# Optimization experiments

Measured on AMD Instinct MI355X. Metric: run time of the kernel, lower is better.

## Reference

```python
import jax, jax.numpy as jnp
import numpy as np

B, L, D = 4, 1024, 512
NST = 16          # d_state
KC = 4            # d_conv
DI = 2 * D        # d_inner (expand=2)
R = (D + 15) // 16  # dt_rank = 32
NM = 4            # mamba instances: 2 layers x (fwd, bwd)


def setup_inputs() -> dict:
    key = jax.random.key(0)
    keys = iter(jax.random.split(key, 64))
    def nrm(shape, s=0.02):
        return jax.random.normal(next(keys), shape, dtype=jnp.float32) * s
    inp = {"x": jax.random.normal(next(keys), (B, L, D), dtype=jnp.float32)}
    # 4 Mamba instances stacked: [layer0_fwd, layer0_bwd, layer1_fwd, layer1_bwd]
    inp["mamba_in_w"] = nrm((NM, 2 * DI, D)); inp["mamba_in_b"] = jnp.zeros((NM, 2 * DI), jnp.float32)
    inp["mamba_conv_w"] = nrm((NM, DI, KC), 0.1); inp["mamba_conv_b"] = jnp.zeros((NM, DI), jnp.float32)
    inp["mamba_xproj_w"] = nrm((NM, R + 2 * NST, DI))
    inp["mamba_dt_w"] = nrm((NM, DI, R)); inp["mamba_dt_b"] = jnp.full((NM, DI), -4.6, jnp.float32)  # softplus -> dt ~ 0.01
    A = jnp.tile(jnp.arange(1, NST + 1, dtype=jnp.float32)[None, :], (DI, 1))  # S4D-real init
    inp["mamba_A_log"] = jnp.tile(jnp.log(A)[None], (NM, 1, 1))
    inp["mamba_D"] = jnp.ones((NM, DI), jnp.float32)
    inp["mamba_out_w"] = nrm((NM, D, DI)); inp["mamba_out_b"] = jnp.zeros((NM, D), jnp.float32)
    # per-BiMambaBlock LayerNorm + FFN params (2 layers)
    inp["ln_w"] = jnp.ones((2, D), jnp.float32); inp["ln_b"] = jnp.zeros((2, D), jnp.float32)
    inp["ffn_ln_w"] = jnp.ones((2, D), jnp.float32); inp["ffn_ln_b"] = jnp.zeros((2, D), jnp.float32)
    inp["ffn_w1"] = nrm((2, 4 * D, D)); inp["ffn_b1"] = jnp.zeros((2, 4 * D), jnp.float32)
    inp["ffn_w2"] = nrm((2, D, 4 * D)); inp["ffn_b2"] = jnp.zeros((2, D), jnp.float32)
    # local conv branches (kernel sizes 5, 7)
    for k in (5, 7):
        inp[f"loc{k}_pw1_w"] = nrm((D, D)); inp[f"loc{k}_pw1_b"] = jnp.zeros((D,), jnp.float32)
        inp[f"loc{k}_dw_w"] = nrm((D, k), 0.1)
        inp[f"loc{k}_pw2_w"] = nrm((D, D)); inp[f"loc{k}_pw2_b"] = jnp.zeros((D,), jnp.float32)
    inp["proj_w"] = nrm((D, 3 * D)); inp["proj_b"] = jnp.zeros((D,), jnp.float32)
    return inp


def _layernorm(x, w, b):
    m = x.mean(-1, keepdims=True)
    v = jnp.var(x, axis=-1, keepdims=True)
    return (x - m) * jax.lax.rsqrt(v + 1e-5) * w + b


def _mamba(u, in_w, in_b, conv_w, conv_b, xp_w, dt_w, dt_b, A_log, Dpar, out_w, out_b):
    # u: [B, L, D]
    xz = u @ in_w.T + in_b
    xm, z = jnp.split(xz, 2, axis=-1)  # each [B, L, DI]
    # causal depthwise conv1d (kernel KC, left pad KC-1) + SiLU
    xt = jnp.swapaxes(xm, 1, 2)  # [B, DI, L]
    xt = jax.lax.conv_general_dilated(xt, conv_w[:, None, :], (1,), [(KC - 1, 0)],
                                      feature_group_count=DI) + conv_b[None, :, None]
    xm = jax.nn.silu(jnp.swapaxes(xt, 1, 2))
    xdb = xm @ xp_w.T  # [B, L, R+2N]
    dt = jax.nn.softplus(xdb[..., :R] @ dt_w.T + dt_b)  # [B, L, DI]
    Bm = xdb[..., R:R + NST]   # [B, L, N]
    Cm = xdb[..., R + NST:]    # [B, L, N]
    A = -jnp.exp(A_log)        # [DI, N]

    def step(h, inp):
        dt_t, B_t, C_t, x_t = inp  # [B,DI],[B,N],[B,N],[B,DI]
        h = h * jnp.exp(dt_t[..., None] * A) + (dt_t * x_t)[..., None] * B_t[:, None, :]
        y = jnp.einsum('bdn,bn->bd', h, C_t)
        return h, y

    h0 = jnp.zeros((u.shape[0], DI, NST), u.dtype)
    xs = (jnp.moveaxis(dt, 1, 0), jnp.moveaxis(Bm, 1, 0),
          jnp.moveaxis(Cm, 1, 0), jnp.moveaxis(xm, 1, 0))
    _, ys = jax.lax.scan(step, h0, xs)  # ys: [L, B, DI]
    y = jnp.moveaxis(ys, 0, 1) + xm * Dpar
    y = y * jax.nn.silu(z)
    return y @ out_w.T + out_b


def _instnorm(h):
    # h: [B, C, L]; InstanceNorm1d default (affine=False, eps=1e-5)
    m = h.mean(-1, keepdims=True)
    v = jnp.var(h, axis=-1, keepdims=True)
    return (h - m) * jax.lax.rsqrt(v + 1e-5)


def _local(x, pw1_w, pw1_b, dw_w, pw2_w, pw2_b, k):
    ht = jnp.swapaxes(x, 1, 2)  # [B, D, L]
    h = jnp.einsum('bcl,dc->bdl', ht, pw1_w) + pw1_b[None, :, None]
    h = jax.nn.silu(_instnorm(h))
    h = jax.lax.conv_general_dilated(h, dw_w[:, None, :], (1,), [(k // 2, k // 2)],
                                     feature_group_count=D)
    h = jax.nn.silu(_instnorm(h))
    h = jnp.einsum('bcl,dc->bdl', h, pw2_w) + pw2_b[None, :, None]
    return jnp.swapaxes(h, 1, 2)


def _forward(x, mamba_in_w, mamba_in_b, mamba_conv_w, mamba_conv_b, mamba_xproj_w,
             mamba_dt_w, mamba_dt_b, mamba_A_log, mamba_D, mamba_out_w, mamba_out_b,
             ln_w, ln_b, ffn_ln_w, ffn_ln_b, ffn_w1, ffn_b1, ffn_w2, ffn_b2,
             loc5_pw1_w, loc5_pw1_b, loc5_dw_w, loc5_pw2_w, loc5_pw2_b,
             loc7_pw1_w, loc7_pw1_b, loc7_dw_w, loc7_pw2_w, loc7_pw2_b,
             proj_w, proj_b):
    mp = (mamba_in_w, mamba_in_b, mamba_conv_w, mamba_conv_b, mamba_xproj_w,
          mamba_dt_w, mamba_dt_b, mamba_A_log, mamba_D, mamba_out_w, mamba_out_b)
    g = x
    for i in range(2):  # num_mamba_layers BiMambaBlocks
        xn = _layernorm(g, ln_w[i], ln_b[i])
        y_fwd = _mamba(xn, *(p[2 * i] for p in mp))
        y_bwd = jnp.flip(_mamba(jnp.flip(xn, 1), *(p[2 * i + 1] for p in mp)), 1)
        g = g + 0.5 * (y_fwd + y_bwd)  # bidir_fusion='mean', residual
        hn = _layernorm(g, ffn_ln_w[i], ffn_ln_b[i])
        h = jax.nn.gelu(hn @ ffn_w1[i].T + ffn_b1[i], approximate=False) @ ffn_w2[i].T + ffn_b2[i]
        g = g + h
    l5 = _local(x, loc5_pw1_w, loc5_pw1_b, loc5_dw_w, loc5_pw2_w, loc5_pw2_b, 5)
    l7 = _local(x, loc7_pw1_w, loc7_pw1_b, loc7_dw_w, loc7_pw2_w, loc7_pw2_b, 7)
    out = jnp.concatenate([g, l5, l7], axis=-1) @ proj_w.T + proj_b  # concat_proj
    return out + x  # lss_residual


def reference(x, mamba_in_w, mamba_in_b, mamba_conv_w, mamba_conv_b, mamba_xproj_w,
              mamba_dt_w, mamba_dt_b, mamba_A_log, mamba_D, mamba_out_w, mamba_out_b,
              ln_w, ln_b, ffn_ln_w, ffn_ln_b, ffn_w1, ffn_b1, ffn_w2, ffn_b2,
              loc5_pw1_w, loc5_pw1_b, loc5_dw_w, loc5_pw2_w, loc5_pw2_b,
              loc7_pw1_w, loc7_pw1_b, loc7_dw_w, loc7_pw2_w, loc7_pw2_b,
              proj_w, proj_b):
    return _forward(x, mamba_in_w, mamba_in_b, mamba_conv_w, mamba_conv_b, mamba_xproj_w,
                    mamba_dt_w, mamba_dt_b, mamba_A_log, mamba_D, mamba_out_w, mamba_out_b,
                    ln_w, ln_b, ffn_ln_w, ffn_ln_b, ffn_w1, ffn_b1, ffn_w2, ffn_b2,
                    loc5_pw1_w, loc5_pw1_b, loc5_dw_w, loc5_pw2_w, loc5_pw2_b,
                    loc7_pw1_w, loc7_pw1_b, loc7_dw_w, loc7_pw2_w, loc7_pw2_b,
                    proj_w, proj_b)
```

## Files before the change

kernel.cpp:

```cpp
#include <hip/hip_runtime.h>
#include <hip/hip_bf16.h>
#include <math.h>

#define BB 4
#define LL 1024
#define DD 512
#define DI 1024
#define NST 16

typedef unsigned short ushort_t;
typedef __attribute__((ext_vector_type(8))) short short8;
typedef __attribute__((ext_vector_type(4))) float f32x4;
typedef __attribute__((ext_vector_type(4))) unsigned short ushort4_t;

__device__ __forceinline__ float silu_f(float x) { return x / (1.f + __expf(-x)); }

__device__ __forceinline__ ushort_t f2bf(float f) {
  union { float f; unsigned u; } v; v.f = f;
  unsigned r = v.u + 0x7fffu + ((v.u >> 16) & 1u);
  return (ushort_t)(r >> 16);
}
__device__ __forceinline__ float bf2f(ushort_t h) {
  union { unsigned u; float f; } v; v.u = ((unsigned)h) << 16;
  return v.f;
}

__device__ __forceinline__ void gl_lds16(const ushort_t* src, ushort_t* dst) {
  __builtin_amdgcn_global_load_lds(
      (const __attribute__((address_space(1))) void*)src,
      (__attribute__((address_space(3))) void*)dst, 16, 0, 0);
}

template <int BN, int ACT, int BIASM, int CMODE, int FLIPA, int FLIPC, int OUTBF, int SPLITK>
__global__ __launch_bounds__(256) void mgemm(
    const ushort_t* __restrict__ A, const ushort_t* __restrict__ Bt,
    const float* __restrict__ bias, void* __restrict__ Cv,
    int K, int lda, int ldb, int ldc, int nreal,
    long sA, long sB, long sC, long sBias, float scale) {
  constexpr int MREP = (BN == 128) ? 4 : 2;
  constexpr int WM = MREP * 16;
  constexpr int NB = BN / 32;
  __shared__ ushort_t As[2][128 * 64];
  __shared__ ushort_t Bs[2][BN * 64];
  const int zz = blockIdx.z;
  const int zdir = (SPLITK == 2) ? (zz >> 2) : zz;
  const ushort_t* Ab;
  const ushort_t* Bb;
  if (SPLITK == 1) {
    Ab = A + (long)zz * K;
    Bb = Bt + (long)zz * K;
  } else if (SPLITK == 2) {
    Ab = A + zdir * sA + (long)(zz & 3) * K;
    Bb = Bt + zdir * sB;
  } else {
    Ab = A + zz * sA;
    Bb = Bt + zz * sB;
  }
  const float* biasp = bias + (long)zdir * sBias;
  const bool flipA = (FLIPA == 1) || (FLIPA == 2 && zdir == 1);
  const bool flipC = (FLIPC == 1) || (FLIPC == 2 && zdir == 1);
  const int flat = blockIdx.y * gridDim.x + blockIdx.x;
  const int nwg = gridDim.x * gridDim.y;
  const int id2 = (flat & 7) * (nwg >> 3) + (flat >> 3);
  const int bm = (id2 / gridDim.x) * 128;
  const int bn = (id2 % gridDim.x) * BN;
  const int tid = threadIdx.x;
  const int wave = tid >> 6, lane = tid & 63;
  const int rlo = lane & 15, q = lane >> 4;
  const int wr = (BN == 128) ? (wave >> 1) : wave;
  const int wc = (BN == 128) ? (wave & 1) : 0;

  f32x4 zero4 = {0.f, 0.f, 0.f, 0.f};
  f32x4 acc[MREP][4];
#pragma unroll
  for (int m = 0; m < MREP; ++m)
#pragma unroll
    for (int n = 0; n < 4; ++n) acc[m][n] = zero4;

  const int srow_off = lane >> 3;
  const int sslot = lane & 7;

#define STAGE_T(bb, k0)                                          \
  do {                                                           \
    _Pragma("unroll") for (int it = 0; it < 4; ++it) {           \
      int c = wave * 4 + it;                                     \
      int row = c * 8 + srow_off;                                \
      int gcol = ((sslot ^ (row & 7)) << 3);                     \
      int gra = bm + row;                                        \
      if (flipA) gra ^= 1023;                                    \
      gl_lds16(Ab + (long)gra * lda + (k0) + gcol, &As[bb][c * 512]); } \
    _Pragma("unroll") for (int it = 0; it < NB; ++it) {          \
      int c = wave * NB + it;                                    \
      int row = c * 8 + srow_off;                                \
      int gcol = ((sslot ^ (row & 7)) << 3);                     \
      gl_lds16(Bb + (long)(bn + row) * ldb + (k0) + gcol, &Bs[bb][c * 512]); } \
  } while (0)

  const int nt = K >> 6;
  STAGE_T(0, 0);
  __syncthreads();
  int cur = 0;
  for (int t = 0; t < nt; ++t) {
    if (t + 1 < nt) STAGE_T(cur ^ 1, (t + 1) * 64);
#pragma unroll
    for (int ks = 0; ks < 2; ++ks) {
      short8 af[MREP], bf[4];
#pragma unroll
      for (int m = 0; m < MREP; ++m) {
        int row = wr * WM + m * 16 + rlo;
        int ch = (ks * 4 + q) ^ (row & 7);
        af[m] = *(const short8*)&As[cur][row * 64 + ch * 8];
      }
#pragma unroll
      for (int n = 0; n < 4; ++n) {
        int row = wc * 64 + n * 16 + rlo;
        int ch = (ks * 4 + q) ^ (row & 7);
        bf[n] = *(const short8*)&Bs[cur][row * 64 + ch * 8];
      }
#pragma unroll
      for (int m = 0; m < MREP; ++m)
#pragma unroll
        for (int n = 0; n < 4; ++n)
          acc[m][n] = __builtin_amdgcn_mfma_f32_16x16x32_bf16(af[m], bf[n], acc[m][n], 0, 0, 0);
    }
    __syncthreads();
    cur ^= 1;
  }
#undef STAGE_T

#pragma unroll
  for (int m = 0; m < MREP; ++m) {
#pragma unroll
    for (int n = 0; n < 4; ++n) {
      int col = bn + wc * 64 + n * 16 + rlo;
      bool cok = (col < nreal);
#pragma unroll
      for (int j = 0; j < 4; ++j) {
        int row = bm + wr * WM + m * 16 + q * 4 + j;
        int orow = flipC ? (row ^ 1023) : row;
        float v = acc[m][n][j];
        if (SPLITK != 1 || zz == 0) {
          if (BIASM == 1) v += biasp[col];
          else if (BIASM == 2) v += biasp[row];
        }
        if (ACT == 1) v = silu_f(v);
        else if (ACT == 2) v = 0.5f * v * (1.f + erff(v * 0.70710678118654752f));
        else if (ACT == 3) v = (v > 20.f) ? v : log1pf(__expf(v));
        if (cok) {
          if (OUTBF) {
            ushort_t* C = (ushort_t*)Cv + (long)zz * sC;
            C[(long)orow * ldc + col] = f2bf(scale * v);
          } else {
            float* C = (float*)Cv + (long)zz * sC;
            if (CMODE == 1) C[(long)orow * ldc + col] += scale * v;
            else C[(long)orow * ldc + col] = scale * v;
          }
        }
      }
    }
  }
}

#define NSEG 10
struct CvtArgs {
  const float* src[NSEG];
  ushort_t* dst[NSEG];
  int start4[NSEG];
};
__global__ __launch_bounds__(256) void cvt_all_kernel(CvtArgs a, int total4) {
  int i = blockIdx.x * 256 + threadIdx.x;
  int stride = gridDim.x * 256;
  for (; i < total4; i += stride) {
    int seg = 0;
#pragma unroll
    for (int s = 1; s < NSEG; ++s)
      if (i >= a.start4[s]) seg = s;
    int off = i - a.start4[seg];
    float4 v = ((const float4*)a.src[seg])[off];
    ushort4_t o;
    o.x = f2bf(v.x); o.y = f2bf(v.y); o.z = f2bf(v.z); o.w = f2bf(v.w);
    *(ushort4_t*)(a.dst[seg] + (long)off * 4) = o;
  }
}

__global__ __launch_bounds__(256) void cvtpad_dtw_kernel(const float* __restrict__ in,
                                                         ushort_t* __restrict__ out) {
  int i = blockIdx.x * 256 + threadIdx.x;
  int k = i & 63;
  int dm = i >> 6;
  out[i] = (k < 32) ? f2bf(in[dm * 32 + k]) : (ushort_t)0;
}

__global__ __launch_bounds__(256) void cvt_kernel(const float* __restrict__ in,
                                                  ushort_t* __restrict__ out, long n) {
  long i = (long)blockIdx.x * 256 + threadIdx.x;
  long stride = (long)gridDim.x * 256;
  for (; i < n; i += stride) out[i] = f2bf(in[i]);
}

__global__ __launch_bounds__(256) void reduce4bf_kernel(const float* __restrict__ p,
                                                        ushort_t* __restrict__ o) {
  int id = blockIdx.x * 256 + threadIdx.x;
  int dir = id >> 16;
  int off = id & 65535;
  const float4* p4 = (const float4*)p + (long)dir * 262144;
  float4 a = p4[off], b = p4[off + 65536], c = p4[off + 131072], d = p4[off + 196608];
  ushort4_t r;
  r.x = f2bf(a.x + b.x + c.x + d.x);
  r.y = f2bf(a.y + b.y + c.y + d.y);
  r.z = f2bf(a.z + b.z + c.z + d.z);
  r.w = f2bf(a.w + b.w + c.w + d.w);
  ((ushort4_t*)o)[(long)dir * 65536 + off] = r;
}

__global__ void transpose_xdb_kernel(const ushort_t* __restrict__ in,
                                     ushort_t* __restrict__ out) {
  __shared__ ushort_t tile[32][33];
  int dir = blockIdx.x >> 7;
  int bl0 = (blockIdx.x & 127) * 32;
  const ushort_t* ip = in + (long)dir * 262144;
  ushort_t* op = out + (long)dir * 131072;
  int tx = threadIdx.x, ty = threadIdx.y;
#pragma unroll
  for (int r = 0; r < 4; ++r)
    tile[ty + 8 * r][tx] = ip[(long)(bl0 + ty + 8 * r) * 64 + 32 + tx];
  __syncthreads();
#pragma unroll
  for (int r = 0; r < 4; ++r)
    op[(long)(ty + 8 * r) * (BB * LL) + bl0 + tx] = tile[tx][ty + 8 * r];
}

__global__ __launch_bounds__(256) void ln_kernel(
    const float* __restrict__ x, const float* __restrict__ w,
    const float* __restrict__ b, ushort_t* __restrict__ o) {
  int row = blockIdx.x * 4 + (threadIdx.x >> 6);
  int lane = threadIdx.x & 63;
  const float* xr = x + (long)row * DD + lane * 8;
  float v[8];
  *(float4*)&v[0] = *(const float4*)&xr[0];
  *(float4*)&v[4] = *(const float4*)&xr[4];
  float s = 0.f, qq = 0.f;
#pragma unroll
  for (int k = 0; k < 8; ++k) { s += v[k]; qq += v[k] * v[k]; }
#pragma unroll
  for (int off = 1; off < 64; off <<= 1) {
    s += __shfl_xor(s, off);
    qq += __shfl_xor(qq, off);
  }
  float mean = s * (1.f / DD);
  float rs = rsqrtf(qq * (1.f / DD) - mean * mean + 1e-5f);
  int c = lane * 8;
  short8 ov;
#pragma unroll
  for (int k = 0; k < 8; ++k)
    ov[k] = (short)f2bf((v[k] - mean) * rs * w[c + k] + b[c + k]);
  *(short8*)&o[(long)row * DD + c] = ov;
}

__global__ __launch_bounds__(256) void inorm_silu_kernel(float* __restrict__ h) {
  long row = blockIdx.x;
  float* p = h + row * (long)LL;
  int t = threadIdx.x;
  float4 v = *(const float4*)&p[t * 4];
  float s = v.x + v.y + v.z + v.w;
  float q = v.x * v.x + v.y * v.y + v.z * v.z + v.w * v.w;
#pragma unroll
  for (int off = 1; off < 64; off <<= 1) {
    s += __shfl_xor(s, off);
    q += __shfl_xor(q, off);
  }
  __shared__ float ss[4], sq[4];
  int wv = t >> 6;
  if ((t & 63) == 0) { ss[wv] = s; sq[wv] = q; }
  __syncthreads();
  s = ss[0] + ss[1] + ss[2] + ss[3];
  q = sq[0] + sq[1] + sq[2] + sq[3];
  float mean = s * (1.f / LL);
  float rs = rsqrtf(q * (1.f / LL) - mean * mean + 1e-5f);
  v.x = silu_f((v.x - mean) * rs);
  v.y = silu_f((v.y - mean) * rs);
  v.z = silu_f((v.z - mean) * rs);
  v.w = silu_f((v.w - mean) * rs);
  *(float4*)&p[t * 4] = v;
}

__global__ __launch_bounds__(256) void mconv_kernel(
    const ushort_t* __restrict__ xz, const float* __restrict__ cw,
    const float* __restrict__ cb, ushort_t* __restrict__ xc) {
  long i = (long)blockIdx.x * 256 + threadIdx.x;
  int dir = (int)(i >> 22);
  long j = i & 4194303;
  int d = (int)(j & (DI - 1));
  long bt = j >> 10;
  int t = (int)(bt & (LL - 1));
  const ushort_t* col = xz + (long)dir * 8388608 + d;
  long r = bt * (2 * DI);
  const float* cwd = cw + dir * 4096;
  float w0 = cwd[d * 4 + 0], w1 = cwd[d * 4 + 1], w2 = cwd[d * 4 + 2], w3 = cwd[d * 4 + 3];
  float acc = cb[dir * 1024 + d];
  if (t >= 3) acc += bf2f(col[r - 3 * 2 * DI]) * w0;
  if (t >= 2) acc += bf2f(col[r - 2 * 2 * DI]) * w1;
  if (t >= 1) acc += bf2f(col[r - 1 * 2 * DI]) * w2;
  acc += bf2f(col[r]) * w3;
  xc[(long)dir * 4194304 + j] = f2bf(silu_f(acc));
}

__global__ void transpose_bf_kernel(const ushort_t* __restrict__ in, ushort_t* __restrict__ out) {
  __shared__ ushort_t tile[32][33];
  int dir = blockIdx.z >> 2;
  int b = blockIdx.z & 3;
  const ushort_t* ip = in + (long)dir * 4194304;
  ushort_t* op = out + (long)dir * 4194304;
  int l0 = blockIdx.x * 32, d0 = blockIdx.y * 32;
  int tx = threadIdx.x, ty = threadIdx.y;
#pragma unroll
  for (int r = 0; r < 4; ++r)
    tile[ty + 8 * r][tx] = ip[((long)b * LL + l0 + ty + 8 * r) * DI + d0 + tx];
  __syncthreads();
#pragma unroll
  for (int r = 0; r < 4; ++r)
    op[(long)(d0 + ty + 8 * r) * (BB * LL) + b * LL + l0 + tx] = tile[tx][ty + 8 * r];
}

__global__ __launch_bounds__(256) void fscan_kernel(
    const ushort_t* __restrict__ dtT, const ushort_t* __restrict__ xcT,
    const ushort_t* __restrict__ xdbT, const float* __restrict__ A_log,
    ushort_t* __restrict__ sT) {
  int wid = (blockIdx.x * 256 + threadIdx.x) >> 6;
  int lane = threadIdx.x & 63;
  int dir = wid >> 12;
  int rest = wid & 4095;
  int b = rest >> 10, d = rest & 1023;

  const ushort_t* dtp = dtT + (long)dir * 4194304;
  const ushort_t* xcp = xcT + (long)dir * 4194304;
  const ushort_t* xbp = xdbT + (long)dir * 131072;
  const float* Alp = A_log + dir * 16384;
  ushort_t* stp = sT + (long)dir * 4194304;

  const long tbase = (long)d * (BB * LL) + b * LL + lane * 16;
  const int blbase = b * LL + lane * 16;

  float dts[16], coef[16], s[16], P[16];
  {
    short8 d0 = *(const short8*)&dtp[tbase];
    short8 d1 = *(const short8*)&dtp[tbase + 8];
    short8 x0 = *(const short8*)&xcp[tbase];
    short8 x1 = *(const short8*)&xcp[tbase + 8];
#pragma unroll
    for (int j = 0; j < 8; ++j) {
      dts[j] = bf2f((ushort_t)d0[j]);
      dts[j + 8] = bf2f((ushort_t)d1[j]);
      coef[j] = dts[j] * bf2f((ushort_t)x0[j]);
      coef[j + 8] = dts[j + 8] * bf2f((ushort_t)x1[j]);
      s[j] = 0.f;
      s[j + 8] = 0.f;
    }
  }

#pragma unroll 1
  for (int n = 0; n < NST; ++n) {
    float Ac = -__expf(Alp[d * NST + n]);
    const ushort_t* Bp = xbp + (long)n * (BB * LL) + blbase;
    const ushort_t* Cp = xbp + (long)(n + 16) * (BB * LL) + blbase;
    short8 b0 = *(const short8*)&Bp[0];
    short8 b1 = *(const short8*)&Bp[8];
    short8 c0 = *(const short8*)&Cp[0];
    short8 c1 = *(const short8*)&Cp[8];
    float h = 0.f, E = 1.f;
#pragma unroll
    for (int t = 0; t < 16; ++t) {
      float e = __expf(Ac * dts[t]);
      float Bv = bf2f((ushort_t)((t < 8) ? b0[t] : b1[t - 8]));
      float Cv = bf2f((ushort_t)((t < 8) ? c0[t] : c1[t - 8]));
      h = h * e + coef[t] * Bv;
      E *= e;
      s[t] = fmaf(h, Cv, s[t]);
      P[t] = E * Cv;
    }
#pragma unroll
    for (int off = 1; off < 64; off <<= 1) {
      float ph = __shfl_up(h, off);
      float pE = __shfl_up(E, off);
      bool ok = lane >= off;
      h = ok ? fmaf(E, ph, h) : h;
      E = ok ? E * pE : E;
    }
    float carry = __shfl_up(h, 1);
    carry = (lane == 0) ? 0.f : carry;
#pragma unroll
    for (int t = 0; t < 16; ++t) s[t] = fmaf(carry, P[t], s[t]);
  }

  short8 o0, o1;
#pragma unroll
  for (int j = 0; j < 8; ++j) {
    o0[j] = (short)f2bf(s[j]);
    o1[j] = (short)f2bf(s[j + 8]);
  }
  *(short8*)&stp[tbase] = o0;
  *(short8*)&stp[tbase + 8] = o1;
}

__global__ void gate_kernel(const ushort_t* __restrict__ sT, const ushort_t* __restrict__ xc,
                            const ushort_t* __restrict__ xz, const float* __restrict__ Dp,
                            ushort_t* __restrict__ y) {
  __shared__ ushort_t tile[32][33];
  int dir = blockIdx.z >> 2;
  int b = blockIdx.z & 3;
  const ushort_t* sp = sT + (long)dir * 4194304;
  const ushort_t* xcp = xc + (long)dir * 4194304;
  const ushort_t* xzp = xz + (long)dir * 8388608;
  const float* Dpd = Dp + dir * 1024;
  ushort_t* yp = y + (long)dir * 4194304;
  int l0 = blockIdx.x * 32, d0 = blockIdx.y * 32;
  int tx = threadIdx.x, ty = threadIdx.y;
#pragma unroll
  for (int r = 0; r < 4; ++r)
    tile[ty + 8 * r][tx] = sp[(long)(d0 + ty + 8 * r) * (BB * LL) + b * LL + l0 + tx];
  __syncthreads();
#pragma unroll
  for (int r = 0; r < 4; ++r) {
    int l = l0 + ty + 8 * r, d = d0 + tx;
    long row = (long)b * LL + l;
    float s = bf2f(tile[tx][ty + 8 * r]);
    float lx = bf2f(xcp[row * DI + d]);
    float zv = bf2f(xzp[row * (2 * DI) + DI + d]);
    yp[row * DI + d] = f2bf((s + lx * Dpd[d]) * silu_f(zv));
  }
}

template <int KW>
__global__ __launch_bounds__(256) void dwconv_kernel(
    const float* __restrict__ in, const float* __restrict__ w, float* __restrict__ out) {
  long i = (long)blockIdx.x * 256 + threadIdx.x;
  int l = (int)(i & (LL - 1));
  long bd = i >> 10;
  int d = (int)(bd & (DD - 1));
  const float* row = in + bd * (long)LL;
  float acc = 0.f;
#pragma unroll
  for (int j = 0; j < KW; ++j) {
    int ll = l + j - KW / 2;
    if (ll >= 0 && ll < LL) acc += row[ll] * w[d * KW + j];
  }
  out[i] = acc;
}

__global__ void transpose_dl_kernel(const float* __restrict__ in, ushort_t* __restrict__ out) {
  __shared__ float tile[32][33];
  int b = blockIdx.z;
  int l0 = blockIdx.x * 32, d0 = blockIdx.y * 32;
  int tx = threadIdx.x, ty = threadIdx.y;
  const float* ib = in + (long)b * DD * LL;
  ushort_t* ob = out + (long)b * LL * DD;
#pragma unroll
  for (int r = 0; r < 4; ++r)
    tile[ty + 8 * r][tx] = ib[(long)(d0 + ty + 8 * r) * LL + l0 + tx];
  __syncthreads();
#pragma unroll
  for (int r = 0; r < 4; ++r)
    ob[(long)(l0 + ty + 8 * r) * DD + d0 + tx] = f2bf(tile[tx][ty + 8 * r]);
}

__global__ __launch_bounds__(256) void copyg_kernel(const float* __restrict__ g,
                                                    ushort_t* __restrict__ cat) {
  long i = (long)blockIdx.x * 256 + threadIdx.x;
  long r = i >> 9;
  int c = (int)(i & 511);
  cat[r * 1536 + c] = f2bf(g[i]);
}

extern "C" void kernel_launch(void* const* d_in, const int* in_sizes, int n_in,
                              void* d_out, int out_size, void* d_ws, size_t ws_size,
                              hipStream_t stream) {
  const float* x        = (const float*)d_in[0];
  const float* in_w     = (const float*)d_in[1];
  const float* in_b     = (const float*)d_in[2];
  const float* conv_w   = (const float*)d_in[3];
  const float* conv_b   = (const float*)d_in[4];
  const float* xp_w     = (const float*)d_in[5];
  const float* dt_w     = (const float*)d_in[6];
  const float* dt_b     = (const float*)d_in[7];
  const float* A_log    = (const float*)d_in[8];
  const float* Dp       = (const float*)d_in[9];
  const float* out_w    = (const float*)d_in[10];
  const float* out_b    = (const float*)d_in[11];
  const float* ln_w     = (const float*)d_in[12];
  const float* ln_b     = (const float*)d_in[13];
  const float* ffn_ln_w = (const float*)d_in[14];
  const float* ffn_ln_b = (const float*)d_in[15];
  const float* ffn_w1   = (const float*)d_in[16];
  const float* ffn_b1   = (const float*)d_in[17];
  const float* ffn_w2   = (const float*)d_in[18];
  const float* ffn_b2   = (const float*)d_in[19];
  const float* l5_pw1w  = (const float*)d_in[20];
  const float* l5_pw1b  = (const float*)d_in[21];
  const float* l5_dww   = (const float*)d_in[22];
  const float* l5_pw2w  = (const float*)d_in[23];
  const float* l5_pw2b  = (const float*)d_in[24];
  const float* l7_pw1w  = (const float*)d_in[25];
  const float* l7_pw1b  = (const float*)d_in[26];
  const float* l7_dww   = (const float*)d_in[27];
  const float* l7_pw2w  = (const float*)d_in[28];
  const float* l7_pw2b  = (const float*)d_in[29];
  const float* proj_w   = (const float*)d_in[30];
  const float* proj_b   = (const float*)d_in[31];
  float* outp = (float*)d_out;

  const long N_BLD = (long)BB * LL * DD;
  ushort_t* wb_in  = (ushort_t*)d_ws;
  ushort_t* wb_out = wb_in + 4194304;
  ushort_t* wb_xp  = wb_out + 2097152;
  ushort_t* wb_dtw = wb_xp + 262144;
  ushort_t* wb_f1  = wb_dtw + 262144;
  ushort_t* wb_f2  = wb_f1 + 2097152;
  ushort_t* wb_pw1 = wb_f2 + 2097152;
  ushort_t* wb_pw2 = wb_pw1 + 524288;
  ushort_t* wb_proj= wb_pw2 + 524288;
  ushort_t* xnb    = wb_proj + 786432;
  float* g = (float*)(xnb + 2097152);
  char* arena = (char*)(g + 2097152);
  ushort_t* xzb = (ushort_t*)arena;
  ushort_t* xcb = xzb + 16777216;
  ushort_t* xcT = xcb + 8388608;
  ushort_t* dtT = xcT + 8388608;
  ushort_t* sT  = dtT + 8388608;
  ushort_t* yb  = sT + 8388608;
  ushort_t* xdb_bf = yb + 8388608;
  float* xdbp = (float*)(xdb_bf + 524288);
  ushort_t* xdbT = (ushort_t*)(xdbp + 2097152);
  ushort_t* h1b = xcT;
  ushort_t* xbf = (ushort_t*)arena;
  float* lh  = (float*)(xbf + 2097152);
  float* lhc = lh + 2097152;
  ushort_t* lhT = (ushort_t*)(lhc + 2097152);
  ushort_t* cat = lhT + 2097152;
  size_t need = (size_t)((char*)(xdbT + 262144) - (char*)d_ws);
  if (ws_size < need) return;

  {
    CvtArgs ca;
    const float* srcs[NSEG] = {in_w, out_w, xp_w, ffn_w1, ffn_w2,
                               l5_pw1w, l7_pw1w, l5_pw2w, l7_pw2w, proj_w};
    ushort_t* dsts[NSEG] = {wb_in, wb_out, wb_xp, wb_f1, wb_f2,
                            wb_pw1, wb_pw1 + 262144, wb_pw2, wb_pw2 + 262144, wb_proj};
    int cnt4[NSEG] = {4194304 / 4, 2097152 / 4, 262144 / 4, 2097152 / 4, 2097152 / 4,
                      262144 / 4, 262144 / 4, 262144 / 4, 262144 / 4, 786432 / 4};
    int acc = 0;
    for (int s = 0; s < NSEG; ++s) { ca.src[s] = srcs[s]; ca.dst[s] = dsts[s]; ca.start4[s] = acc; acc += cnt4[s]; }
    cvt_all_kernel<<<2048, 256, 0, stream>>>(ca, acc);
  }
  cvtpad_dtw_kernel<<<1024, 256, 0, stream>>>(dt_w, wb_dtw);

  hipMemcpyAsync(g, x, N_BLD * 4, hipMemcpyDeviceToDevice, stream);

  const long sBL = (long)LL * DD;
  for (int i = 0; i < 2; ++i) {
    int m0 = 2 * i;
    ln_kernel<<<1024, 256, 0, stream>>>(g, ln_w + i * 512, ln_b + i * 512, xnb);
    mgemm<128, 0, 1, 0, 2, 0, 1, 0><<<dim3(16, 32, 2), 256, 0, stream>>>(
        xnb, wb_in + (long)m0 * 1048576, in_b + (long)m0 * 2048, xzb,
        512, 512, 512, 2048, 2048, 0, 1048576, 8388608, 2048, 1.f);
    mconv_kernel<<<32768, 256, 0, stream>>>(xzb, conv_w + (long)m0 * 4096,
                                            conv_b + (long)m0 * 1024, xcb);
    transpose_bf_kernel<<<dim3(32, 32, 8), dim3(32, 8), 0, stream>>>(xcb, xcT);
    mgemm<64, 0, 0, 0, 0, 0, 0, 2><<<dim3(1, 32, 8), 256, 0, stream>>>(
        xcb, wb_xp + (long)m0 * 65536, nullptr, xdbp, 256, 1024, 1024, 64, 64,
        4194304, 65536, 262144, 0, 1.f);
    reduce4bf_kernel<<<512, 256, 0, stream>>>(xdbp, xdb_bf);
    transpose_xdb_kernel<<<256, dim3(32, 8), 0, stream>>>(xdb_bf, xdbT);
    mgemm<128, 3, 2, 0, 0, 0, 1, 0><<<dim3(32, 8, 2), 256, 0, stream>>>(
        wb_dtw + (long)m0 * 65536, xdb_bf, dt_b + (long)m0 * 1024, dtT,
        64, 64, 64, 4096, 4096, 65536, 262144, 4194304, 1024, 1.f);
    fscan_kernel<<<2048, 256, 0, stream>>>(dtT, xcT, xdbT,
                                           A_log + (long)m0 * 16384, sT);
    gate_kernel<<<dim3(32, 32, 8), dim3(32, 8), 0, stream>>>(
        sT, xcb, xzb, Dp + (long)m0 * 1024, yb);
    mgemm<64, 0, 1, 1, 0, 0, 0, 0><<<dim3(8, 32, 1), 256, 0, stream>>>(
        yb, wb_out + (long)m0 * 524288, out_b + (long)m0 * 512, g,
        1024, 1024, 1024, 512, 512, 0, 0, 0, 0, 0.5f);
    mgemm<64, 0, 1, 1, 0, 1, 0, 0><<<dim3(8, 32, 1), 256, 0, stream>>>(
        yb + 4194304, wb_out + (long)(m0 + 1) * 524288, out_b + (long)(m0 + 1) * 512, g,
        1024, 1024, 1024, 512, 512, 0, 0, 0, 0, 0.5f);
    ln_kernel<<<1024, 256, 0, stream>>>(g, ffn_ln_w + i * 512, ffn_ln_b + i * 512, xnb);
    mgemm<128, 2, 1, 0, 0, 0, 1, 0><<<dim3(16, 32, 1), 256, 0, stream>>>(
        xnb, wb_f1 + (long)i * 1048576, ffn_b1 + (long)i * 2048, h1b,
        512, 512, 512, 2048, 2048, 0, 0, 0, 0, 1.f);
    mgemm<64, 0, 1, 1, 0, 0, 0, 0><<<dim3(8, 32, 1), 256, 0, stream>>>(
        h1b, wb_f2 + (long)i * 1048576, ffn_b2 + (long)i * 512, g,
        2048, 2048, 2048, 512, 512, 0, 0, 0, 0, 1.f);
  }

  cvt_kernel<<<512, 256, 0, stream>>>(x, xbf, N_BLD);
  for (int k = 0; k < 2; ++k) {
    const ushort_t* pw1w = wb_pw1 + (long)k * 262144;
    const float* pw1b = k ? l7_pw1b : l5_pw1b;
    const float* dww  = k ? l7_dww  : l5_dww;
    const ushort_t* pw2w = wb_pw2 + (long)k * 262144;
    const float* pw2b = k ? l7_pw2b : l5_pw2b;
    mgemm<64, 0, 2, 0, 0, 0, 0, 0><<<dim3(16, 4, 4), 256, 0, stream>>>(
        pw1w, xbf, pw1b, lh, 512, 512, 512, 1024, 1024, 0, sBL, sBL, 0, 1.f);
    inorm_silu_kernel<<<2048, 256, 0, stream>>>(lh);
    if (k)
      dwconv_kernel<7><<<8192, 256, 0, stream>>>(lh, dww, lhc);
    else
      dwconv_kernel<5><<<8192, 256, 0, stream>>>(lh, dww, lhc);
    inorm_silu_kernel<<<2048, 256, 0, stream>>>(lhc);
    transpose_dl_kernel<<<dim3(32, 16, 4), dim3(32, 8), 0, stream>>>(lhc, lhT);
    mgemm<64, 0, 1, 0, 0, 0, 1, 0><<<dim3(8, 8, 4), 256, 0, stream>>>(
        lhT, pw2w, pw2b, cat + (k ? 1024 : 512), 512, 512, 512, 1536, 512,
        sBL, 0, (long)LL * 1536, 0, 1.f);
  }
  copyg_kernel<<<8192, 256, 0, stream>>>(g, cat);
  hipMemcpyAsync(outp, x, N_BLD * 4, hipMemcpyDeviceToDevice, stream);
  mgemm<64, 0, 1, 1, 0, 0, 0, 0><<<dim3(8, 32, 1), 256, 0, stream>>>(
      cat, wb_proj, proj_b, outp, 1536, 1536, 1536, 512, 512, 0, 0, 0, 0, 1.f);
}
```

Baseline: 748.7 us.

## Fuse mamba conv with transpose, merge fwd/bwd out-proj GEMMs, fp32 B/C for scan

The depthwise conv and the transpose of its output now run in one tiled kernel, which stages the input in shared memory and writes both layouts, so the extra read pass over xc goes away. The gate kernel writes forward and backward outputs side by side in one concatenated buffer, with the time-reversal flip for the backward direction folded into the store index. The two out-projection GEMMs become one K=2048 GEMM against a concatenated weight and a pre-summed bias built at setup. The scan now reads B/C as fp32 and uses exp2f with a prescaled A, which doubles the B/C bytes read but removes per-element bf16 unpacking.

```diff
diff --git a/kernel.cpp b/kernel.cpp
--- a/kernel.cpp
+++ b/kernel.cpp
@@ -161,7 +161,7 @@
   }
 }
 
-#define NSEG 10
+#define NSEG 9
 struct CvtArgs {
   const float* src[NSEG];
   ushort_t* dst[NSEG];
@@ -180,6 +180,21 @@
     ushort4_t o;
     o.x = f2bf(v.x); o.y = f2bf(v.y); o.z = f2bf(v.z); o.w = f2bf(v.w);
     *(ushort4_t*)(a.dst[seg] + (long)off * 4) = o;
+  }
+}
+
+__global__ __launch_bounds__(256) void cvt_outw_kernel(
+    const float* __restrict__ w, const float* __restrict__ bsrc,
+    ushort_t* __restrict__ wo, float* __restrict__ bo) {
+  int i = blockIdx.x * 256 + threadIdx.x;
+  int c = i & 2047;
+  int r = (i >> 11) & 511;
+  int layer = i >> 20;
+  int m = layer * 2 + (c >> 10);
+  wo[i] = f2bf(w[(long)m * 524288 + r * 1024 + (c & 1023)]);
+  if (i < 1024) {
+    int ly = i >> 9, rr = i & 511;
+    bo[i] = bsrc[(ly * 2) * 512 + rr] + bsrc[(ly * 2 + 1) * 512 + rr];
   }
 }
 
@@ -214,16 +229,16 @@
 }
 
 __global__ void transpose_xdb_kernel(const ushort_t* __restrict__ in,
-                                     ushort_t* __restrict__ out) {
-  __shared__ ushort_t tile[32][33];
+                                     float* __restrict__ out) {
+  __shared__ float tile[32][33];
   int dir = blockIdx.x >> 7;
   int bl0 = (blockIdx.x & 127) * 32;
   const ushort_t* ip = in + (long)dir * 262144;
-  ushort_t* op = out + (long)dir * 131072;
+  float* op = out + (long)dir * 131072;
   int tx = threadIdx.x, ty = threadIdx.y;
 #pragma unroll
   for (int r = 0; r < 4; ++r)
-    tile[ty + 8 * r][tx] = ip[(long)(bl0 + ty + 8 * r) * 64 + 32 + tx];
+    tile[ty + 8 * r][tx] = bf2f(ip[(long)(bl0 + ty + 8 * r) * 64 + 32 + tx]);
   __syncthreads();
 #pragma unroll
   for (int r = 0; r < 4; ++r)
@@ -284,47 +299,49 @@
   *(float4*)&p[t * 4] = v;
 }
 
-__global__ __launch_bounds__(256) void mconv_kernel(
-    const ushort_t* __restrict__ xz, const float* __restrict__ cw,
-    const float* __restrict__ cb, ushort_t* __restrict__ xc) {
-  long i = (long)blockIdx.x * 256 + threadIdx.x;
-  int dir = (int)(i >> 22);
-  long j = i & 4194303;
-  int d = (int)(j & (DI - 1));
-  long bt = j >> 10;
-  int t = (int)(bt & (LL - 1));
-  const ushort_t* col = xz + (long)dir * 8388608 + d;
-  long r = bt * (2 * DI);
-  const float* cwd = cw + dir * 4096;
-  float w0 = cwd[d * 4 + 0], w1 = cwd[d * 4 + 1], w2 = cwd[d * 4 + 2], w3 = cwd[d * 4 + 3];
-  float acc = cb[dir * 1024 + d];
-  if (t >= 3) acc += bf2f(col[r - 3 * 2 * DI]) * w0;
-  if (t >= 2) acc += bf2f(col[r - 2 * 2 * DI]) * w1;
-  if (t >= 1) acc += bf2f(col[r - 1 * 2 * DI]) * w2;
-  acc += bf2f(col[r]) * w3;
-  xc[(long)dir * 4194304 + j] = f2bf(silu_f(acc));
-}
-
-__global__ void transpose_bf_kernel(const ushort_t* __restrict__ in, ushort_t* __restrict__ out) {
-  __shared__ ushort_t tile[32][33];
-  int dir = blockIdx.z >> 2;
-  int b = blockIdx.z & 3;
-  const ushort_t* ip = in + (long)dir * 4194304;
-  ushort_t* op = out + (long)dir * 4194304;
+__global__ void mconvt_kernel(const ushort_t* __restrict__ xz, const float* __restrict__ cw,
+                              const float* __restrict__ cb, ushort_t* __restrict__ xc,
+                              ushort_t* __restrict__ xcT) {
+  __shared__ float raw[35][32];
+  __shared__ ushort_t ot[32][33];
+  int dirb = blockIdx.z;
+  int dir = dirb >> 2, b = dirb & 3;
   int l0 = blockIdx.x * 32, d0 = blockIdx.y * 32;
   int tx = threadIdx.x, ty = threadIdx.y;
+  const ushort_t* xzp = xz + (long)dir * 8388608;
+  int tid = ty * 32 + tx;
+  for (int e = tid; e < 35 * 32; e += 256) {
+    int rr = e >> 5, cc = e & 31;
+    int l = l0 - 3 + rr;
+    float v = 0.f;
+    if (l >= 0) v = bf2f(xzp[((long)b * LL + l) * 2048 + d0 + cc]);
+    raw[rr][cc] = v;
+  }
+  __syncthreads();
+  int d = d0 + tx;
+  const float* cwd = cw + dir * 4096 + d * 4;
+  float w0 = cwd[0], w1 = cwd[1], w2 = cwd[2], w3 = cwd[3];
+  float bias = cb[dir * 1024 + d];
+  ushort_t* xcp = xc + (long)dir * 4194304;
+#pragma unroll
+  for (int r = 0; r < 4; ++r) {
+    int li = ty + 8 * r;
+    float acc = bias + raw[li][tx] * w0 + raw[li + 1][tx] * w1 +
+                raw[li + 2][tx] * w2 + raw[li + 3][tx] * w3;
+    ushort_t bfv = f2bf(silu_f(acc));
+    xcp[((long)b * LL + l0 + li) * DI + d] = bfv;
+    ot[li][tx] = bfv;
+  }
+  __syncthreads();
+  ushort_t* xtp = xcT + (long)dir * 4194304;
 #pragma unroll
   for (int r = 0; r < 4; ++r)
-    tile[ty + 8 * r][tx] = ip[((long)b * LL + l0 + ty + 8 * r) * DI + d0 + tx];
-  __syncthreads();
-#pragma unroll
-  for (int r = 0; r < 4; ++r)
-    op[(long)(d0 + ty + 8 * r) * (BB * LL) + b * LL + l0 + tx] = tile[tx][ty + 8 * r];
+    xtp[(long)(d0 + ty + 8 * r) * (BB * LL) + b * LL + l0 + tx] = ot[tx][ty + 8 * r];
 }
 
 __global__ __launch_bounds__(256) void fscan_kernel(
     const ushort_t* __restrict__ dtT, const ushort_t* __restrict__ xcT,
-    const ushort_t* __restrict__ xdbT, const float* __restrict__ A_log,
+    const float* __restrict__ xdbT, const float* __restrict__ A_log,
     ushort_t* __restrict__ sT) {
   int wid = (blockIdx.x * 256 + threadIdx.x) >> 6;
   int lane = threadIdx.x & 63;
@@ -334,7 +351,7 @@
 
   const ushort_t* dtp = dtT + (long)dir * 4194304;
   const ushort_t* xcp = xcT + (long)dir * 4194304;
-  const ushort_t* xbp = xdbT + (long)dir * 131072;
+  const float* xbp = xdbT + (long)dir * 131072;
   const float* Alp = A_log + dir * 16384;
   ushort_t* stp = sT + (long)dir * 4194304;
 
@@ -360,19 +377,21 @@
 
 #pragma unroll 1
   for (int n = 0; n < NST; ++n) {
-    float Ac = -__expf(Alp[d * NST + n]);
-    const ushort_t* Bp = xbp + (long)n * (BB * LL) + blbase;
-    const ushort_t* Cp = xbp + (long)(n + 16) * (BB * LL) + blbase;
-    short8 b0 = *(const short8*)&Bp[0];
-    short8 b1 = *(const short8*)&Bp[8];
-    short8 c0 = *(const short8*)&Cp[0];
-    short8 c1 = *(const short8*)&Cp[8];
+    float Ac2 = -__expf(Alp[d * NST + n]) * 1.44269504f;
+    const float* Bp = xbp + n * (BB * LL) + blbase;
+    const float* Cp = xbp + (n + 16) * (BB * LL) + blbase;
+    f32x4 B4[4], C4[4];
+#pragma unroll
+    for (int k = 0; k < 4; ++k) {
+      B4[k] = ((const f32x4*)Bp)[k];
+      C4[k] = ((const f32x4*)Cp)[k];
+    }
     float h = 0.f, E = 1.f;
 #pragma unroll
     for (int t = 0; t < 16; ++t) {
-      float e = __expf(Ac * dts[t]);
-      float Bv = bf2f((ushort_t)((t < 8) ? b0[t] : b1[t - 8]));
-      float Cv = bf2f((ushort_t)((t < 8) ? c0[t] : c1[t - 8]));
+      float e = exp2f(Ac2 * dts[t]);
+      float Bv = B4[t >> 2][t & 3];
+      float Cv = C4[t >> 2][t & 3];
       h = h * e + coef[t] * Bv;
       E *= e;
       s[t] = fmaf(h, Cv, s[t]);
@@ -404,7 +423,7 @@
 
 __global__ void gate_kernel(const ushort_t* __restrict__ sT, const ushort_t* __restrict__ xc,
                             const ushort_t* __restrict__ xz, const float* __restrict__ Dp,
-                            ushort_t* __restrict__ y) {
+                            ushort_t* __restrict__ yc) {
   __shared__ ushort_t tile[32][33];
   int dir = blockIdx.z >> 2;
   int b = blockIdx.z & 3;
@@ -412,7 +431,6 @@
   const ushort_t* xcp = xc + (long)dir * 4194304;
   const ushort_t* xzp = xz + (long)dir * 8388608;
   const float* Dpd = Dp + dir * 1024;
-  ushort_t* yp = y + (long)dir * 4194304;
   int l0 = blockIdx.x * 32, d0 = blockIdx.y * 32;
   int tx = threadIdx.x, ty = threadIdx.y;
 #pragma unroll
@@ -426,7 +444,8 @@
     float s = bf2f(tile[tx][ty + 8 * r]);
     float lx = bf2f(xcp[row * DI + d]);
     float zv = bf2f(xzp[row * (2 * DI) + DI + d]);
-    yp[row * DI + d] = f2bf((s + lx * Dpd[d]) * silu_f(zv));
+    long orow = dir ? (row ^ 1023) : row;
+    yc[orow * 2048 + dir * 1024 + d] = f2bf((s + lx * Dpd[d]) * silu_f(zv));
   }
 }
 
@@ -509,16 +528,17 @@
   float* outp = (float*)d_out;
 
   const long N_BLD = (long)BB * LL * DD;
-  ushort_t* wb_in  = (ushort_t*)d_ws;
-  ushort_t* wb_out = wb_in + 4194304;
-  ushort_t* wb_xp  = wb_out + 2097152;
-  ushort_t* wb_dtw = wb_xp + 262144;
-  ushort_t* wb_f1  = wb_dtw + 262144;
-  ushort_t* wb_f2  = wb_f1 + 2097152;
-  ushort_t* wb_pw1 = wb_f2 + 2097152;
-  ushort_t* wb_pw2 = wb_pw1 + 524288;
-  ushort_t* wb_proj= wb_pw2 + 524288;
-  ushort_t* xnb    = wb_proj + 786432;
+  ushort_t* wb_in   = (ushort_t*)d_ws;
+  ushort_t* wb_out2 = wb_in + 4194304;
+  ushort_t* wb_xp   = wb_out2 + 2097152;
+  ushort_t* wb_dtw  = wb_xp + 262144;
+  ushort_t* wb_f1   = wb_dtw + 262144;
+  ushort_t* wb_f2   = wb_f1 + 2097152;
+  ushort_t* wb_pw1  = wb_f2 + 2097152;
+  ushort_t* wb_pw2  = wb_pw1 + 524288;
+  ushort_t* wb_proj = wb_pw2 + 524288;
+  float* ob2 = (float*)(wb_proj + 786432);
+  ushort_t* xnb = (ushort_t*)(ob2 + 1024);
   float* g = (float*)(xnb + 2097152);
   char* arena = (char*)(g + 2097152);
   ushort_t* xzb = (ushort_t*)arena;
@@ -526,10 +546,10 @@
   ushort_t* xcT = xcb + 8388608;
   ushort_t* dtT = xcT + 8388608;
   ushort_t* sT  = dtT + 8388608;
-  ushort_t* yb  = sT + 8388608;
-  ushort_t* xdb_bf = yb + 8388608;
+  ushort_t* yc  = sT + 8388608;
+  ushort_t* xdb_bf = yc + 8388608;
   float* xdbp = (float*)(xdb_bf + 524288);
-  ushort_t* xdbT = (ushort_t*)(xdbp + 2097152);
+  float* xdbT = xdbp + 2097152;
   ushort_t* h1b = xcT;
   ushort_t* xbf = (ushort_t*)arena;
   float* lh  = (float*)(xbf + 2097152);
@@ -541,16 +561,17 @@
 
   {
     CvtArgs ca;
-    const float* srcs[NSEG] = {in_w, out_w, xp_w, ffn_w1, ffn_w2,
+    const float* srcs[NSEG] = {in_w, xp_w, ffn_w1, ffn_w2,
                                l5_pw1w, l7_pw1w, l5_pw2w, l7_pw2w, proj_w};
-    ushort_t* dsts[NSEG] = {wb_in, wb_out, wb_xp, wb_f1, wb_f2,
+    ushort_t* dsts[NSEG] = {wb_in, wb_xp, wb_f1, wb_f2,
                             wb_pw1, wb_pw1 + 262144, wb_pw2, wb_pw2 + 262144, wb_proj};
-    int cnt4[NSEG] = {4194304 / 4, 2097152 / 4, 262144 / 4, 2097152 / 4, 2097152 / 4,
+    int cnt4[NSEG] = {4194304 / 4, 262144 / 4, 2097152 / 4, 2097152 / 4,
                       262144 / 4, 262144 / 4, 262144 / 4, 262144 / 4, 786432 / 4};
     int acc = 0;
     for (int s = 0; s < NSEG; ++s) { ca.src[s] = srcs[s]; ca.dst[s] = dsts[s]; ca.start4[s] = acc; acc += cnt4[s]; }
     cvt_all_kernel<<<2048, 256, 0, stream>>>(ca, acc);
   }
+  cvt_outw_kernel<<<8192, 256, 0, stream>>>(out_w, out_b, wb_out2, ob2);
   cvtpad_dtw_kernel<<<1024, 256, 0, stream>>>(dt_w, wb_dtw);
 
   hipMemcpyAsync(g, x, N_BLD * 4, hipMemcpyDeviceToDevice, stream);
@@ -562,9 +583,8 @@
     mgemm<128, 0, 1, 0, 2, 0, 1, 0><<<dim3(16, 32, 2), 256, 0, stream>>>(
         xnb, wb_in + (long)m0 * 1048576, in_b + (long)m0 * 2048, xzb,
         512, 512, 512, 2048, 2048, 0, 1048576, 8388608, 2048, 1.f);
-    mconv_kernel<<<32768, 256, 0, stream>>>(xzb, conv_w + (long)m0 * 4096,
-                                            conv_b + (long)m0 * 1024, xcb);
-    transpose_bf_kernel<<<dim3(32, 32, 8), dim3(32, 8), 0, stream>>>(xcb, xcT);
+    mconvt_kernel<<<dim3(32, 32, 8), dim3(32, 8), 0, stream>>>(
+        xzb, conv_w + (long)m0 * 4096, conv_b + (long)m0 * 1024, xcb, xcT);
     mgemm<64, 0, 0, 0, 0, 0, 0, 2><<<dim3(1, 32, 8), 256, 0, stream>>>(
         xcb, wb_xp + (long)m0 * 65536, nullptr, xdbp, 256, 1024, 1024, 64, 64,
         4194304, 65536, 262144, 0, 1.f);
@@ -576,13 +596,10 @@
     fscan_kernel<<<2048, 256, 0, stream>>>(dtT, xcT, xdbT,
                                            A_log + (long)m0 * 16384, sT);
     gate_kernel<<<dim3(32, 32, 8), dim3(32, 8), 0, stream>>>(
-        sT, xcb, xzb, Dp + (long)m0 * 1024, yb);
+        sT, xcb, xzb, Dp + (long)m0 * 1024, yc);
     mgemm<64, 0, 1, 1, 0, 0, 0, 0><<<dim3(8, 32, 1), 256, 0, stream>>>(
-        yb, wb_out + (long)m0 * 524288, out_b + (long)m0 * 512, g,
-        1024, 1024, 1024, 512, 512, 0, 0, 0, 0, 0.5f);
-    mgemm<64, 0, 1, 1, 0, 1, 0, 0><<<dim3(8, 32, 1), 256, 0, stream>>>(
-        yb + 4194304, wb_out + (long)(m0 + 1) * 524288, out_b + (long)(m0 + 1) * 512, g,
-        1024, 1024, 1024, 512, 512, 0, 0, 0, 0, 0.5f);
+        yc, wb_out2 + (long)i * 1048576, ob2 + i * 512, g,
+        2048, 2048, 2048, 512, 512, 0, 0, 0, 0, 0.5f);
     ln_kernel<<<1024, 256, 0, stream>>>(g, ffn_ln_w + i * 512, ffn_ln_b + i * 512, xnb);
     mgemm<128, 2, 1, 0, 0, 0, 1, 0><<<dim3(16, 32, 1), 256, 0, stream>>>(
         xnb, wb_f1 + (long)i * 1048576, ffn_b1 + (long)i * 2048, h1b,
```

New measurement: 747.5 us. Within noise of the previous version (-0.2%).
